# Performance work log

Measured on AMD Instinct MI355X. Metric: run time of the kernel, lower is better.

Reference implementation:

```python
import jax, jax.numpy as jnp
import numpy as np

N, H, W, C, CK, ITER = 4, 256, 256, 8, 2, 4
HID = 2 * C
C2 = C * C


def project(x, w1, b1, w2, b2, w3, b3):
    # flax Project: Dense->gelu->Dense->gelu->Dense (gelu approximate=tanh, jax default)
    h = jax.nn.gelu(x @ w1 + b1)
    h = jax.nn.gelu(h @ w2 + b2)
    return h @ w3 + b3


def setup_inputs() -> dict:
    key = jax.random.key(0)
    ks = jax.random.split(key, 40)
    d = {}
    d['u'] = jax.random.normal(ks[0], (N, H, W, C), jnp.float32)
    d['k'] = jax.random.normal(ks[1], (N, H, W, CK), jnp.float32)
    idx = 2
    # gamma MLP (in CK), delta MLP (in CK), greens real/imag MLPs (in 2)
    for nm, fin in zip(['g', 'dl', 'fr', 'fi'], [CK, CK, 2, 2]):
        for li, (fi_, fo) in enumerate([(fin, HID), (HID, HID), (HID, C2)]):
            d[f'{nm}_w{li+1}'] = jax.random.normal(ks[idx], (fi_, fo), jnp.float32) / np.sqrt(fi_).astype(np.float32)
            d[f'{nm}_b{li+1}'] = jnp.zeros((fo,), jnp.float32)
            idx += 1
    d['bias'] = jax.random.normal(ks[idx], (C,), jnp.float32)
    return d


def reference(u, k, g_w1, g_b1, g_w2, g_b2, g_w3, g_b3,
              dl_w1, dl_b1, dl_w2, dl_b2, dl_w3, dl_b3,
              fr_w1, fr_b1, fr_w2, fr_b2, fr_w3, fr_b3,
              fi_w1, fi_b1, fi_w2, fi_b2, fi_w3, fi_b3, bias):
    # per-pixel gamma / delta matrices: (N,H,W,C,C), scaled by 1/C^2 as in original
    gmat = (project(k, g_w1, g_b1, g_w2, g_b2, g_w3, g_b3) / C2).reshape(N, H, W, C, C)
    dmat = (project(k, dl_w1, dl_b1, dl_w2, dl_b2, dl_w3, dl_b3) / C2).reshape(N, H, W, C, C)
    # spectral Green's filter on the rfft grid; meshgrid(kx, ky) -> (W, H//2+1)
    kx = jnp.fft.rfftfreq(H, d=1.0 / H)
    ky = jnp.fft.fftfreq(W, d=1.0 / W)
    Kx, Ky = jnp.meshgrid(kx, ky)
    K = jnp.stack([Kx, Ky], axis=-1).astype(jnp.float32)  # (W, H//2+1, 2)
    filt_r = project(K, fr_w1, fr_b1, fr_w2, fr_b2, fr_w3, fr_b3)
    filt_i = project(K, fi_w1, fi_b1, fi_w2, fi_b2, fi_w3, fi_b3)
    filt = ((filt_r + 1j * filt_i) / C2).reshape(W, H // 2 + 1, C, C)  # H==W
    for _ in range(ITER):
        local = 2.0 * u - jnp.einsum('nhwj,nhwjk->nhwk', u, gmat)
        du = jnp.einsum('nhwj,nhwjk->nhwk', u, dmat)
        uf = jnp.fft.rfftn(du, axes=(1, 2))  # (N,H,W//2+1,C) complex
        gu = jnp.fft.irfftn(jnp.einsum('nhwj,hwjk->nhwk', uf, filt), axes=(1, 2))
        u = local + jnp.einsum('nhwj,nhwjk->nhwk', gu, gmat)
    return jax.nn.gelu(u + bias)
```

## Files before the change

### kernel.cpp

```cpp
#include <hip/hip_runtime.h>
#include <math.h>

#define NB 4
#define HB 256
#define WB 256
#define CB 8
#define NPIX (NB*HB*WB)
#define W2B 129
#define TWO_PI_F 6.283185307179586f

__device__ __forceinline__ float gelu_f(float x){
    float z = 0.7978845608028654f*(x + 0.044715f*x*x*x);
    return x / (1.0f + __expf(-2.0f*z));
}

__device__ __forceinline__ unsigned pack_bf16x2(float a, float b){
    unsigned ua = __float_as_uint(a), ub = __float_as_uint(b);
    ua = (ua + 0x7FFFu + ((ua >> 16) & 1u)) >> 16;
    ub = (ub + 0x7FFFu + ((ub >> 16) & 1u)) >> 16;
    return ua | (ub << 16);
}
__device__ __forceinline__ float2 unpack_bf16x2(unsigned v){
    return make_float2(__uint_as_float(v << 16), __uint_as_float(v & 0xFFFF0000u));
}

__device__ __forceinline__ void ldcp(float* dst, const float* __restrict__ src, int n, int t){
    for (int i = t; i < n; i += 256) dst[i] = src[i];
}

__global__ __launch_bounds__(256) void prep_kernel(
    const float* __restrict__ kin,
    const float* gw1,const float* gb1,const float* gw2,const float* gb2,const float* gw3,const float* gb3,
    const float* dw1,const float* db1,const float* dw2,const float* db2,const float* dw3,const float* db3,
    const float* fw1,const float* fb1,const float* fw2,const float* fb2,const float* fw3,const float* fb3,
    const float* iw1,const float* ib1,const float* iw2,const float* ib2,const float* iw3,const float* ib3,
    unsigned* __restrict__ gmat, unsigned* __restrict__ dmat,
    unsigned* __restrict__ fpack)
{
    __shared__ float sw[2816];
    int t = threadIdx.x;
    int b = blockIdx.x;
    if (b < 1024){
        int gd = (b >= 512);
        const float* w1 = gd ? dw1 : gw1;  const float* b1 = gd ? db1 : gb1;
        const float* w2 = gd ? dw2 : gw2;  const float* b2 = gd ? db2 : gb2;
        const float* w3 = gd ? dw3 : gw3;  const float* b3 = gd ? db3 : gb3;
        ldcp(sw+0,   w1,  32, t); ldcp(sw+32,  b1, 16, t);
        ldcp(sw+48,  w2, 256, t); ldcp(sw+304, b2, 16, t);
        ldcp(sw+320, w3,1024, t); ldcp(sw+1344,b3, 64, t);
        __syncthreads();
        unsigned* mat = gd ? dmat : gmat;
        int bb_ = b & 511;
        float a[2], bv[2]; size_t base[2];
#pragma unroll
        for (int p = 0; p < 2; ++p){
            int pix = bb_*512 + p*256 + t;
            float2 kv = ((const float2*)kin)[pix];
            a[p] = kv.x; bv[p] = kv.y;
            base[p] = (size_t)(pix >> 6)*2048 + (pix & 63);
        }
        float h1[2][16], h2[2][16];
#pragma unroll
        for (int o = 0; o < 16; ++o){
            float wx = sw[o], wy = sw[16+o], bo = sw[32+o];
#pragma unroll
            for (int p = 0; p < 2; ++p) h1[p][o] = gelu_f(a[p]*wx + bv[p]*wy + bo);
        }
#pragma unroll
        for (int o = 0; o < 16; ++o){
            float acc0 = sw[304+o], acc1 = acc0;
#pragma unroll
            for (int i = 0; i < 16; ++i){
                float w = sw[48+i*16+o];
                acc0 += h1[0][i]*w; acc1 += h1[1][i]*w;
            }
            h2[0][o] = gelu_f(acc0); h2[1][o] = gelu_f(acc1);
        }
        const float s = 1.0f/64.0f;
#pragma unroll
        for (int o = 0; o < 64; o += 2){
            float a0[2], a1[2];
#pragma unroll
            for (int p = 0; p < 2; ++p){ a0[p] = sw[1344+o]; a1[p] = sw[1344+o+1]; }
#pragma unroll
            for (int i = 0; i < 16; ++i){
                float w0 = sw[320+i*64+o], w1v = sw[320+i*64+o+1];
#pragma unroll
                for (int p = 0; p < 2; ++p){ a0[p] += h2[p][i]*w0; a1[p] += h2[p][i]*w1v; }
            }
#pragma unroll
            for (int p = 0; p < 2; ++p)
                mat[base[p] + (size_t)(o>>1)*64] = pack_bf16x2(a0[p]*s, a1[p]*s);
        }
    } else {
        ldcp(sw+0,   fw1,  32, t); ldcp(sw+32,  fb1, 16, t);
        ldcp(sw+48,  fw2, 256, t); ldcp(sw+304, fb2, 16, t);
        ldcp(sw+320, fw3,1024, t); ldcp(sw+1344,fb3, 64, t);
        ldcp(sw+1408+0,   iw1,  32, t); ldcp(sw+1408+32,  ib1, 16, t);
        ldcp(sw+1408+48,  iw2, 256, t); ldcp(sw+1408+304, ib2, 16, t);
        ldcp(sw+1408+320, iw3,1024, t); ldcp(sw+1408+1344,ib3, 64, t);
        __syncthreads();
        int w2 = b - 1024;
        float x = (float)w2;
        float y = (float)(t < 128 ? t : t - 256);
        float h1r[16], h1i[16], h2r[16], h2i[16];
#pragma unroll
        for (int o = 0; o < 16; ++o){
            h1r[o] = gelu_f(x*sw[o] + y*sw[16+o] + sw[32+o]);
            h1i[o] = gelu_f(x*sw[1408+o] + y*sw[1408+16+o] + sw[1408+32+o]);
        }
#pragma unroll
        for (int o = 0; o < 16; ++o){
            float ar = sw[304+o], ai = sw[1408+304+o];
#pragma unroll
            for (int i = 0; i < 16; ++i){
                ar += h1r[i]*sw[48+i*16+o];
                ai += h1i[i]*sw[1408+48+i*16+o];
            }
            h2r[o] = gelu_f(ar); h2i[o] = gelu_f(ai);
        }
        unsigned* dst = fpack + (size_t)w2*16384 + t;
        const float s = 1.0f/64.0f;
#pragma unroll
        for (int o = 0; o < 64; ++o){
            float ar = sw[1344+o], ai = sw[1408+1344+o];
#pragma unroll
            for (int i = 0; i < 16; ++i){
                ar += h2r[i]*sw[320+i*64+o];
                ai += h2i[i]*sw[1408+320+i*64+o];
            }
            dst[o*256] = pack_bf16x2(ar*s, ai*s);
        }
    }
}

template<int CH>
__device__ __forceinline__ void fft256c(float* xr, float* xi, int t, float sgn)
{
    int n2 = t >> 4, k1 = t & 15;
    float csA, snA; __sincosf(sgn*TWO_PI_F*(float)k1*(1.0f/16.0f), &snA, &csA);
    float ar[CH], ai[CH];
#pragma unroll
    for (int c = 0; c < CH; ++c){ ar[c]=0.f; ai[c]=0.f; }
    float cw = 1.f, sw = 0.f;
#pragma unroll
    for (int n1 = 0; n1 < 16; ++n1){
#pragma unroll
        for (int c = 0; c < CH; ++c){
            float xrv = xr[c*256 + 16*n1 + n2];
            float xiv = xi[c*256 + 16*n1 + n2];
            ar[c] += xrv*cw - xiv*sw;
            ai[c] += xrv*sw + xiv*cw;
        }
        float cn = cw*csA - sw*snA;
        sw = cw*snA + sw*csA; cw = cn;
    }
    float cs2, sn2; __sincosf(sgn*TWO_PI_F*(float)(n2*k1)*(1.0f/256.0f), &sn2, &cs2);
#pragma unroll
    for (int c = 0; c < CH; ++c){
        float br = ar[c]*cs2 - ai[c]*sn2;
        float bi = ar[c]*sn2 + ai[c]*cs2;
        ar[c] = br; ai[c] = bi;
    }
    __syncthreads();
#pragma unroll
    for (int c = 0; c < CH; ++c){ xr[c*256+t] = ar[c]; xi[c*256+t] = ai[c]; }
    __syncthreads();
    int k1b = t & 15, k2 = t >> 4;
    float csB, snB; __sincosf(sgn*TWO_PI_F*(float)k2*(1.0f/16.0f), &snB, &csB);
    float yr[CH], yi[CH];
#pragma unroll
    for (int c = 0; c < CH; ++c){ yr[c]=0.f; yi[c]=0.f; }
    cw = 1.f; sw = 0.f;
#pragma unroll
    for (int n2b = 0; n2b < 16; ++n2b){
#pragma unroll
        for (int c = 0; c < CH; ++c){
            float br = xr[c*256 + n2b*16 + k1b];
            float bi = xi[c*256 + n2b*16 + k1b];
            yr[c] += br*cw - bi*sw;
            yi[c] += br*sw + bi*cw;
        }
        float cn = cw*csB - sw*snB;
        sw = cw*snB + sw*csB; cw = cn;
    }
    __syncthreads();
#pragma unroll
    for (int c = 0; c < CH; ++c){ xr[c*256+t] = yr[c]; xi[c*256+t] = yi[c]; }
    __syncthreads();
}

__device__ __forceinline__ void fwd_pack_fft_store(
    float* xr, float* xi, const float* dv, int t, int n, int h,
    float2* __restrict__ spec)
{
#pragma unroll
    for (int c2 = 0; c2 < 4; ++c2){ xr[c2*256+t] = dv[2*c2]; xi[c2*256+t] = dv[2*c2+1]; }
    __syncthreads();
    fft256c<4>(xr, xi, t, -1.f);
    if (t <= 128){
        int m = (256 - t) & 255;
        float4* dst = (float4*)(spec + (((size_t)n*129 + t)*256 + h)*8);
#pragma unroll
        for (int c2 = 0; c2 < 4; ++c2){
            float Zr = xr[c2*256+t], Zi = xi[c2*256+t];
            float Yr = xr[c2*256+m], Yi = xi[c2*256+m];
            dst[c2] = make_float4(0.5f*(Zr+Yr), 0.5f*(Zi-Yi),
                                  0.5f*(Zi+Yi), 0.5f*(Yr-Zr));
        }
    }
}

__device__ __forceinline__ void inv_fft_to_gu(
    const float2* __restrict__ spec, float* xr, float* xi,
    float (*sre)[132], float (*sim)[132], int t, int n, int h, float* gu)
{
    for (int idx = t; idx < 129*8; idx += 256){
        int w2 = idx >> 3, c = idx & 7;
        float2 v = spec[(((size_t)n*129 + w2)*256 + h)*8 + c];
        sre[c][w2] = v.x; sim[c][w2] = v.y;
    }
    __syncthreads();
#pragma unroll
    for (int c2 = 0; c2 < 4; ++c2){
        int a = 2*c2, b = 2*c2+1;
        if (t <= 128){
            xr[c2*256+t] = sre[a][t] - sim[b][t];
            xi[c2*256+t] = sim[a][t] + sre[b][t];
        } else {
            int m = 256 - t;
            xr[c2*256+t] =  sre[a][m] + sim[b][m];
            xi[c2*256+t] = -sim[a][m] + sre[b][m];
        }
    }
    __syncthreads();
    fft256c<4>(xr, xi, t, +1.f);
    const float s = 1.0f/65536.0f;
#pragma unroll
    for (int c2 = 0; c2 < 4; ++c2){
        gu[2*c2]   = xr[c2*256+t]*s;
        gu[2*c2+1] = xi[c2*256+t]*s;
    }
}

__global__ __launch_bounds__(256) void fft_fwd_kernel(
    const float* __restrict__ u, const unsigned* __restrict__ dmat,
    float2* __restrict__ spec)
{
    __shared__ float xr[4][256], xi[4][256];
    int t = threadIdx.x, bid = blockIdx.x;
    int n = bid >> 8, h = bid & 255;
    const float* up = u + (size_t)bid*2048 + (size_t)t*8;
    float4 ua = ((const float4*)up)[0], ub = ((const float4*)up)[1];
    float uv[8] = {ua.x,ua.y,ua.z,ua.w, ub.x,ub.y,ub.z,ub.w};
    const unsigned* dp = dmat + ((size_t)bid*4 + (t>>6))*2048 + (t&63);
    float dv[8];
#pragma unroll
    for (int k = 0; k < 8; ++k) dv[k] = 0.f;
#pragma unroll
    for (int j = 0; j < 8; ++j){
        float uj = uv[j];
#pragma unroll
        for (int k2 = 0; k2 < 4; ++k2){
            float2 f = unpack_bf16x2(dp[(j*4+k2)*64]);
            dv[2*k2]   += uj * f.x;
            dv[2*k2+1] += uj * f.y;
        }
    }
    fwd_pack_fft_store(&xr[0][0], &xi[0][0], dv, t, n, h, spec);
}

__global__ __launch_bounds__(512) void ffth_mult_kernel(
    float2* __restrict__ spec, const unsigned* __restrict__ fpack)
{
    __shared__ float xr[8][256], xi[8][256];
    int tid = threadIdx.x;
    int t = tid & 255, g = tid >> 8;
    int c0 = g*4;
    int n = blockIdx.x / 129, w2 = blockIdx.x % 129;
    float2* base = spec + ((size_t)(n*129 + w2))*2048;
    const float4* rp = (const float4*)(base + (size_t)t*8);
    float4 ra = rp[g*2], rb = rp[g*2+1];
    xr[c0+0][t]=ra.x; xi[c0+0][t]=ra.y; xr[c0+1][t]=ra.z; xi[c0+1][t]=ra.w;
    xr[c0+2][t]=rb.x; xi[c0+2][t]=rb.y; xr[c0+3][t]=rb.z; xi[c0+3][t]=rb.w;
    __syncthreads();
    fft256c<4>(&xr[c0][0], &xi[c0][0], t, -1.f);

    float sr[8], si[8];
#pragma unroll
    for (int j = 0; j < 8; ++j){ sr[j] = xr[j][t]; si[j] = xi[j][t]; }
    float orr[4], oii[4];
#pragma unroll
    for (int kq = 0; kq < 4; ++kq){ orr[kq]=0.f; oii[kq]=0.f; }
    const unsigned* fp = fpack + (size_t)w2*16384 + t;
#pragma unroll
    for (int j = 0; j < 8; ++j){
        float sjr = sr[j], sji = si[j];
#pragma unroll
        for (int kq = 0; kq < 4; ++kq){
            float2 f = unpack_bf16x2(fp[(j*8 + c0 + kq)*256]);
            orr[kq] += sjr*f.x - sji*f.y;
            oii[kq] += sjr*f.y + sji*f.x;
        }
    }
    __syncthreads();
#pragma unroll
    for (int kq = 0; kq < 4; ++kq){ xr[c0+kq][t] = orr[kq]; xi[c0+kq][t] = oii[kq]; }
    __syncthreads();
    fft256c<4>(&xr[c0][0], &xi[c0][0], t, +1.f);
    float4* wp = (float4*)(base + (size_t)t*8);
    wp[g*2]   = make_float4(xr[c0+0][t], xi[c0+0][t], xr[c0+1][t], xi[c0+1][t]);
    wp[g*2+1] = make_float4(xr[c0+2][t], xi[c0+2][t], xr[c0+3][t], xi[c0+3][t]);
}

__global__ __launch_bounds__(256) void born_step_kernel(
    float2* __restrict__ spec, const float* __restrict__ u_in,
    float* __restrict__ u_out, const unsigned* __restrict__ gmat,
    const unsigned* __restrict__ dmat)
{
    __shared__ float sre[8][132], sim[8][132];
    __shared__ float xr[4][256], xi[4][256];
    int t = threadIdx.x, bid = blockIdx.x;
    int n = bid >> 8, h = bid & 255;
    float gu[8];
    inv_fft_to_gu(spec, &xr[0][0], &xi[0][0], sre, sim, t, n, h, gu);

    const float* up = u_in + (size_t)bid*2048 + (size_t)t*8;
    float4 ua = ((const float4*)up)[0], ub = ((const float4*)up)[1];
    float uv[8] = {ua.x,ua.y,ua.z,ua.w, ub.x,ub.y,ub.z,ub.w};
    float e[8], acc[8];
#pragma unroll
    for (int c = 0; c < 8; ++c){ e[c] = gu[c] - uv[c]; acc[c] = 2.0f*uv[c]; }
    const unsigned* gp = gmat + ((size_t)bid*4 + (t>>6))*2048 + (t&63);
#pragma unroll
    for (int j = 0; j < 8; ++j){
        float ej = e[j];
#pragma unroll
        for (int k2 = 0; k2 < 4; ++k2){
            float2 f = unpack_bf16x2(gp[(j*4+k2)*64]);
            acc[2*k2]   += ej * f.x;
            acc[2*k2+1] += ej * f.y;
        }
    }
    float* op = u_out + (size_t)bid*2048 + (size_t)t*8;
    ((float4*)op)[0] = make_float4(acc[0],acc[1],acc[2],acc[3]);
    ((float4*)op)[1] = make_float4(acc[4],acc[5],acc[6],acc[7]);

    const unsigned* dp = dmat + ((size_t)bid*4 + (t>>6))*2048 + (t&63);
    float dv[8];
#pragma unroll
    for (int k = 0; k < 8; ++k) dv[k] = 0.f;
#pragma unroll
    for (int j = 0; j < 8; ++j){
        float uj = acc[j];
#pragma unroll
        for (int k2 = 0; k2 < 4; ++k2){
            float2 f = unpack_bf16x2(dp[(j*4+k2)*64]);
            dv[2*k2]   += uj * f.x;
            dv[2*k2+1] += uj * f.y;
        }
    }
    fwd_pack_fft_store(&xr[0][0], &xi[0][0], dv, t, n, h, spec);
}

__global__ __launch_bounds__(256) void final_kernel(
    const float2* __restrict__ spec, const float* __restrict__ u_in,
    const unsigned* __restrict__ gmat, const float* __restrict__ bias,
    float* __restrict__ out)
{
    __shared__ float sre[8][132], sim[8][132];
    __shared__ float xr[4][256], xi[4][256];
    int t = threadIdx.x, bid = blockIdx.x;
    int n = bid >> 8, h = bid & 255;
    float gu[8];
    inv_fft_to_gu(spec, &xr[0][0], &xi[0][0], sre, sim, t, n, h, gu);

    const float* up = u_in + (size_t)bid*2048 + (size_t)t*8;
    float4 ua = ((const float4*)up)[0], ub = ((const float4*)up)[1];
    float uv[8] = {ua.x,ua.y,ua.z,ua.w, ub.x,ub.y,ub.z,ub.w};
    float e[8], acc[8];
#pragma unroll
    for (int c = 0; c < 8; ++c){ e[c] = gu[c] - uv[c]; acc[c] = 2.0f*uv[c]; }
    const unsigned* gp = gmat + ((size_t)bid*4 + (t>>6))*2048 + (t&63);
#pragma unroll
    for (int j = 0; j < 8; ++j){
        float ej = e[j];
#pragma unroll
        for (int k2 = 0; k2 < 4; ++k2){
            float2 f = unpack_bf16x2(gp[(j*4+k2)*64]);
            acc[2*k2]   += ej * f.x;
            acc[2*k2+1] += ej * f.y;
        }
    }
#pragma unroll
    for (int k = 0; k < 8; ++k) acc[k] = gelu_f(acc[k] + bias[k]);
    float* op = out + (size_t)bid*2048 + (size_t)t*8;
    ((float4*)op)[0] = make_float4(acc[0],acc[1],acc[2],acc[3]);
    ((float4*)op)[1] = make_float4(acc[4],acc[5],acc[6],acc[7]);
}

extern "C" void kernel_launch(void* const* d_in, const int* in_sizes, int n_in,
                              void* d_out, int out_size, void* d_ws, size_t ws_size,
                              hipStream_t stream) {
    const float* u_in = (const float*)d_in[0];
    const float* k_in = (const float*)d_in[1];
    const float* Wp[24];
    for (int i = 0; i < 24; ++i) Wp[i] = (const float*)d_in[2+i];
    const float* bias = (const float*)d_in[26];

    char* base = (char*)d_ws;
    unsigned* gmat  = (unsigned*)(base);
    unsigned* dmat  = (unsigned*)(base + 33554432ull);
    unsigned* fpack = (unsigned*)(base + 67108864ull);
    float*    u_ws  = (float*)   (base + 75563008ull);
    float2*   spec  = (float2*)  (base + 83951616ull);

    prep_kernel<<<1153, 256, 0, stream>>>(k_in,
        Wp[0],Wp[1],Wp[2],Wp[3],Wp[4],Wp[5],
        Wp[6],Wp[7],Wp[8],Wp[9],Wp[10],Wp[11],
        Wp[12],Wp[13],Wp[14],Wp[15],Wp[16],Wp[17],
        Wp[18],Wp[19],Wp[20],Wp[21],Wp[22],Wp[23],
        gmat, dmat, fpack);

    fft_fwd_kernel<<<1024, 256, 0, stream>>>(u_in, dmat, spec);
    for (int it = 0; it < 4; ++it){
        ffth_mult_kernel<<<516, 512, 0, stream>>>(spec, fpack);
        if (it < 3){
            born_step_kernel<<<1024, 256, 0, stream>>>(
                spec, (it == 0) ? u_in : u_ws, u_ws, gmat, dmat);
        } else {
            final_kernel<<<1024, 256, 0, stream>>>(spec, u_ws, gmat, bias, (float*)d_out);
        }
    }
}
```

Measured before the change: 240.6 us.

## Interleave FFT channels in shared memory as float4 vectors and load spectra directly

Shared-memory FFT buffers change from channel-major scalar arrays to pixel-major float4 vectors. Each butterfly step then reads and writes four channels with a single 128-bit LDS access instead of four scalar ones. The inverse path also drops the staging sre/sim arrays and one barrier: each thread loads its mirrored spectrum entry directly as four float4s. The 128-bit strided LDS reads may hit more bank conflicts, and the mirrored global loads are less coalesced.

```diff
diff --git a/kernel.cpp b/kernel.cpp
--- a/kernel.cpp
+++ b/kernel.cpp
@@ -8,6 +8,8 @@
 #define NPIX (NB*HB*WB)
 #define W2B 129
 #define TWO_PI_F 6.283185307179586f
+
+typedef float f32x4 __attribute__((ext_vector_type(4)));
 
 __device__ __forceinline__ float gelu_f(float x){
     float z = 0.7978845608028654f*(x + 0.044715f*x*x*x);
@@ -134,120 +136,91 @@
     }
 }
 
-template<int CH>
-__device__ __forceinline__ void fft256c(float* xr, float* xi, int t, float sgn)
+__device__ __forceinline__ void fft256v(f32x4* xr, f32x4* xi, int t, float sgn)
 {
     int n2 = t >> 4, k1 = t & 15;
     float csA, snA; __sincosf(sgn*TWO_PI_F*(float)k1*(1.0f/16.0f), &snA, &csA);
-    float ar[CH], ai[CH];
-#pragma unroll
-    for (int c = 0; c < CH; ++c){ ar[c]=0.f; ai[c]=0.f; }
+    f32x4 ar = {0.f,0.f,0.f,0.f}, ai = {0.f,0.f,0.f,0.f};
     float cw = 1.f, sw = 0.f;
 #pragma unroll
     for (int n1 = 0; n1 < 16; ++n1){
-#pragma unroll
-        for (int c = 0; c < CH; ++c){
-            float xrv = xr[c*256 + 16*n1 + n2];
-            float xiv = xi[c*256 + 16*n1 + n2];
-            ar[c] += xrv*cw - xiv*sw;
-            ai[c] += xrv*sw + xiv*cw;
-        }
+        f32x4 vr = xr[16*n1 + n2], vi = xi[16*n1 + n2];
+        ar += vr*cw - vi*sw;
+        ai += vr*sw + vi*cw;
         float cn = cw*csA - sw*snA;
         sw = cw*snA + sw*csA; cw = cn;
     }
     float cs2, sn2; __sincosf(sgn*TWO_PI_F*(float)(n2*k1)*(1.0f/256.0f), &sn2, &cs2);
-#pragma unroll
-    for (int c = 0; c < CH; ++c){
-        float br = ar[c]*cs2 - ai[c]*sn2;
-        float bi = ar[c]*sn2 + ai[c]*cs2;
-        ar[c] = br; ai[c] = bi;
-    }
-    __syncthreads();
-#pragma unroll
-    for (int c = 0; c < CH; ++c){ xr[c*256+t] = ar[c]; xi[c*256+t] = ai[c]; }
+    f32x4 br = ar*cs2 - ai*sn2;
+    f32x4 bi = ar*sn2 + ai*cs2;
+    __syncthreads();
+    xr[t] = br; xi[t] = bi;
     __syncthreads();
     int k1b = t & 15, k2 = t >> 4;
     float csB, snB; __sincosf(sgn*TWO_PI_F*(float)k2*(1.0f/16.0f), &snB, &csB);
-    float yr[CH], yi[CH];
-#pragma unroll
-    for (int c = 0; c < CH; ++c){ yr[c]=0.f; yi[c]=0.f; }
+    f32x4 yr = {0.f,0.f,0.f,0.f}, yi = {0.f,0.f,0.f,0.f};
     cw = 1.f; sw = 0.f;
 #pragma unroll
     for (int n2b = 0; n2b < 16; ++n2b){
-#pragma unroll
-        for (int c = 0; c < CH; ++c){
-            float br = xr[c*256 + n2b*16 + k1b];
-            float bi = xi[c*256 + n2b*16 + k1b];
-            yr[c] += br*cw - bi*sw;
-            yi[c] += br*sw + bi*cw;
-        }
+        f32x4 br2 = xr[n2b*16 + k1b], bi2 = xi[n2b*16 + k1b];
+        yr += br2*cw - bi2*sw;
+        yi += br2*sw + bi2*cw;
         float cn = cw*csB - sw*snB;
         sw = cw*snB + sw*csB; cw = cn;
     }
     __syncthreads();
-#pragma unroll
-    for (int c = 0; c < CH; ++c){ xr[c*256+t] = yr[c]; xi[c*256+t] = yi[c]; }
-    __syncthreads();
-}
-
-__device__ __forceinline__ void fwd_pack_fft_store(
-    float* xr, float* xi, const float* dv, int t, int n, int h,
+    xr[t] = yr; xi[t] = yi;
+    __syncthreads();
+}
+
+__device__ __forceinline__ void fwd_store(
+    f32x4* XR, f32x4* XI, const float* dv, int t, int n, int h,
     float2* __restrict__ spec)
 {
-#pragma unroll
-    for (int c2 = 0; c2 < 4; ++c2){ xr[c2*256+t] = dv[2*c2]; xi[c2*256+t] = dv[2*c2+1]; }
-    __syncthreads();
-    fft256c<4>(xr, xi, t, -1.f);
+    XR[t] = (f32x4){dv[0],dv[2],dv[4],dv[6]};
+    XI[t] = (f32x4){dv[1],dv[3],dv[5],dv[7]};
+    __syncthreads();
+    fft256v(XR, XI, t, -1.f);
     if (t <= 128){
         int m = (256 - t) & 255;
+        f32x4 zr = XR[t], zi = XI[t], yr = XR[m], yi = XI[m];
         float4* dst = (float4*)(spec + (((size_t)n*129 + t)*256 + h)*8);
-#pragma unroll
-        for (int c2 = 0; c2 < 4; ++c2){
-            float Zr = xr[c2*256+t], Zi = xi[c2*256+t];
-            float Yr = xr[c2*256+m], Yi = xi[c2*256+m];
-            dst[c2] = make_float4(0.5f*(Zr+Yr), 0.5f*(Zi-Yi),
-                                  0.5f*(Zi+Yi), 0.5f*(Yr-Zr));
-        }
+        dst[0] = make_float4(0.5f*(zr.x+yr.x), 0.5f*(zi.x-yi.x), 0.5f*(zi.x+yi.x), 0.5f*(yr.x-zr.x));
+        dst[1] = make_float4(0.5f*(zr.y+yr.y), 0.5f*(zi.y-yi.y), 0.5f*(zi.y+yi.y), 0.5f*(yr.y-zr.y));
+        dst[2] = make_float4(0.5f*(zr.z+yr.z), 0.5f*(zi.z-yi.z), 0.5f*(zi.z+yi.z), 0.5f*(yr.z-zr.z));
+        dst[3] = make_float4(0.5f*(zr.w+yr.w), 0.5f*(zi.w-yi.w), 0.5f*(zi.w+yi.w), 0.5f*(yr.w-zr.w));
     }
 }
 
 __device__ __forceinline__ void inv_fft_to_gu(
-    const float2* __restrict__ spec, float* xr, float* xi,
-    float (*sre)[132], float (*sim)[132], int t, int n, int h, float* gu)
-{
-    for (int idx = t; idx < 129*8; idx += 256){
-        int w2 = idx >> 3, c = idx & 7;
-        float2 v = spec[(((size_t)n*129 + w2)*256 + h)*8 + c];
-        sre[c][w2] = v.x; sim[c][w2] = v.y;
-    }
-    __syncthreads();
-#pragma unroll
-    for (int c2 = 0; c2 < 4; ++c2){
-        int a = 2*c2, b = 2*c2+1;
-        if (t <= 128){
-            xr[c2*256+t] = sre[a][t] - sim[b][t];
-            xi[c2*256+t] = sim[a][t] + sre[b][t];
-        } else {
-            int m = 256 - t;
-            xr[c2*256+t] =  sre[a][m] + sim[b][m];
-            xi[c2*256+t] = -sim[a][m] + sre[b][m];
-        }
-    }
-    __syncthreads();
-    fft256c<4>(xr, xi, t, +1.f);
+    const float2* __restrict__ spec, f32x4* XR, f32x4* XI,
+    int t, int n, int h, float* gu)
+{
+    int w2 = (t <= 128) ? t : 256 - t;
+    const float4* rp = (const float4*)(spec + (((size_t)n*129 + w2)*256 + h)*8);
+    float4 q0 = rp[0], q1 = rp[1], q2 = rp[2], q3 = rp[3];
+    f32x4 xr, xi;
+    if (t <= 128){
+        xr = (f32x4){q0.x - q0.w, q1.x - q1.w, q2.x - q2.w, q3.x - q3.w};
+        xi = (f32x4){q0.y + q0.z, q1.y + q1.z, q2.y + q2.z, q3.y + q3.z};
+    } else {
+        xr = (f32x4){ q0.x + q0.w,  q1.x + q1.w,  q2.x + q2.w,  q3.x + q3.w};
+        xi = (f32x4){-q0.y + q0.z, -q1.y + q1.z, -q2.y + q2.z, -q3.y + q3.z};
+    }
+    XR[t] = xr; XI[t] = xi;
+    __syncthreads();
+    fft256v(XR, XI, t, +1.f);
     const float s = 1.0f/65536.0f;
-#pragma unroll
-    for (int c2 = 0; c2 < 4; ++c2){
-        gu[2*c2]   = xr[c2*256+t]*s;
-        gu[2*c2+1] = xi[c2*256+t]*s;
-    }
+    f32x4 gr = XR[t], gi = XI[t];
+    gu[0]=gr.x*s; gu[1]=gi.x*s; gu[2]=gr.y*s; gu[3]=gi.y*s;
+    gu[4]=gr.z*s; gu[5]=gi.z*s; gu[6]=gr.w*s; gu[7]=gi.w*s;
 }
 
 __global__ __launch_bounds__(256) void fft_fwd_kernel(
     const float* __restrict__ u, const unsigned* __restrict__ dmat,
     float2* __restrict__ spec)
 {
-    __shared__ float xr[4][256], xi[4][256];
+    __shared__ f32x4 XR[256], XI[256];
     int t = threadIdx.x, bid = blockIdx.x;
     int n = bid >> 8, h = bid & 255;
     const float* up = u + (size_t)bid*2048 + (size_t)t*8;
@@ -267,13 +240,13 @@
             dv[2*k2+1] += uj * f.y;
         }
     }
-    fwd_pack_fft_store(&xr[0][0], &xi[0][0], dv, t, n, h, spec);
+    fwd_store(XR, XI, dv, t, n, h, spec);
 }
 
 __global__ __launch_bounds__(512) void ffth_mult_kernel(
     float2* __restrict__ spec, const unsigned* __restrict__ fpack)
 {
-    __shared__ float xr[8][256], xi[8][256];
+    __shared__ f32x4 XR[2][256], XI[2][256];
     int tid = threadIdx.x;
     int t = tid & 255, g = tid >> 8;
     int c0 = g*4;
@@ -281,36 +254,36 @@
     float2* base = spec + ((size_t)(n*129 + w2))*2048;
     const float4* rp = (const float4*)(base + (size_t)t*8);
     float4 ra = rp[g*2], rb = rp[g*2+1];
-    xr[c0+0][t]=ra.x; xi[c0+0][t]=ra.y; xr[c0+1][t]=ra.z; xi[c0+1][t]=ra.w;
-    xr[c0+2][t]=rb.x; xi[c0+2][t]=rb.y; xr[c0+3][t]=rb.z; xi[c0+3][t]=rb.w;
-    __syncthreads();
-    fft256c<4>(&xr[c0][0], &xi[c0][0], t, -1.f);
-
-    float sr[8], si[8];
-#pragma unroll
-    for (int j = 0; j < 8; ++j){ sr[j] = xr[j][t]; si[j] = xi[j][t]; }
-    float orr[4], oii[4];
-#pragma unroll
-    for (int kq = 0; kq < 4; ++kq){ orr[kq]=0.f; oii[kq]=0.f; }
+    XR[g][t] = (f32x4){ra.x, ra.z, rb.x, rb.z};
+    XI[g][t] = (f32x4){ra.y, ra.w, rb.y, rb.w};
+    __syncthreads();
+    fft256v(XR[g], XI[g], t, -1.f);
+
+    f32x4 s0r = XR[0][t], s1r = XR[1][t], s0i = XI[0][t], s1i = XI[1][t];
+    float sr[8] = {s0r.x,s0r.y,s0r.z,s0r.w, s1r.x,s1r.y,s1r.z,s1r.w};
+    float si[8] = {s0i.x,s0i.y,s0i.z,s0i.w, s1i.x,s1i.y,s1i.z,s1i.w};
+    f32x4 orr = {0.f,0.f,0.f,0.f}, oii = {0.f,0.f,0.f,0.f};
     const unsigned* fp = fpack + (size_t)w2*16384 + t;
 #pragma unroll
     for (int j = 0; j < 8; ++j){
         float sjr = sr[j], sji = si[j];
-#pragma unroll
-        for (int kq = 0; kq < 4; ++kq){
-            float2 f = unpack_bf16x2(fp[(j*8 + c0 + kq)*256]);
-            orr[kq] += sjr*f.x - sji*f.y;
-            oii[kq] += sjr*f.y + sji*f.x;
-        }
-    }
-    __syncthreads();
-#pragma unroll
-    for (int kq = 0; kq < 4; ++kq){ xr[c0+kq][t] = orr[kq]; xi[c0+kq][t] = oii[kq]; }
-    __syncthreads();
-    fft256c<4>(&xr[c0][0], &xi[c0][0], t, +1.f);
+        float2 f0 = unpack_bf16x2(fp[(j*8 + c0 + 0)*256]);
+        float2 f1 = unpack_bf16x2(fp[(j*8 + c0 + 1)*256]);
+        float2 f2 = unpack_bf16x2(fp[(j*8 + c0 + 2)*256]);
+        float2 f3 = unpack_bf16x2(fp[(j*8 + c0 + 3)*256]);
+        orr.x += sjr*f0.x - sji*f0.y;  oii.x += sjr*f0.y + sji*f0.x;
+        orr.y += sjr*f1.x - sji*f1.y;  oii.y += sjr*f1.y + sji*f1.x;
+        orr.z += sjr*f2.x - sji*f2.y;  oii.z += sjr*f2.y + sji*f2.x;
+        orr.w += sjr*f3.x - sji*f3.y;  oii.w += sjr*f3.y + sji*f3.x;
+    }
+    __syncthreads();
+    XR[g][t] = orr; XI[g][t] = oii;
+    __syncthreads();
+    fft256v(XR[g], XI[g], t, +1.f);
+    f32x4 vr = XR[g][t], vi = XI[g][t];
     float4* wp = (float4*)(base + (size_t)t*8);
-    wp[g*2]   = make_float4(xr[c0+0][t], xi[c0+0][t], xr[c0+1][t], xi[c0+1][t]);
-    wp[g*2+1] = make_float4(xr[c0+2][t], xi[c0+2][t], xr[c0+3][t], xi[c0+3][t]);
+    wp[g*2]   = make_float4(vr.x, vi.x, vr.y, vi.y);
+    wp[g*2+1] = make_float4(vr.z, vi.z, vr.w, vi.w);
 }
 
 __global__ __launch_bounds__(256) void born_step_kernel(
@@ -318,12 +291,11 @@
     float* __restrict__ u_out, const unsigned* __restrict__ gmat,
     const unsigned* __restrict__ dmat)
 {
-    __shared__ float sre[8][132], sim[8][132];
-    __shared__ float xr[4][256], xi[4][256];
+    __shared__ f32x4 XR[256], XI[256];
     int t = threadIdx.x, bid = blockIdx.x;
     int n = bid >> 8, h = bid & 255;
     float gu[8];
-    inv_fft_to_gu(spec, &xr[0][0], &xi[0][0], sre, sim, t, n, h, gu);
+    inv_fft_to_gu(spec, XR, XI, t, n, h, gu);
 
     const float* up = u_in + (size_t)bid*2048 + (size_t)t*8;
     float4 ua = ((const float4*)up)[0], ub = ((const float4*)up)[1];
@@ -360,7 +332,7 @@
             dv[2*k2+1] += uj * f.y;
         }
     }
-    fwd_pack_fft_store(&xr[0][0], &xi[0][0], dv, t, n, h, spec);
+    fwd_store(XR, XI, dv, t, n, h, spec);
 }
 
 __global__ __launch_bounds__(256) void final_kernel(
@@ -368,12 +340,11 @@
     const unsigned* __restrict__ gmat, const float* __restrict__ bias,
     float* __restrict__ out)
 {
-    __shared__ float sre[8][132], sim[8][132];
-    __shared__ float xr[4][256], xi[4][256];
+    __shared__ f32x4 XR[256], XI[256];
     int t = threadIdx.x, bid = blockIdx.x;
     int n = bid >> 8, h = bid & 255;
     float gu[8];
-    inv_fft_to_gu(spec, &xr[0][0], &xi[0][0], sre, sim, t, n, h, gu);
+    inv_fft_to_gu(spec, XR, XI, t, n, h, gu);
 
     const float* up = u_in + (size_t)bid*2048 + (size_t)t*8;
     float4 ua = ((const float4*)up)[0], ub = ((const float4*)up)[1];
```

Result: faster. 231.7 us (-3.7%).
